# Kernel optimization log

Hardware: AMD Instinct MI355X
Metric: run time of the kernel (lower is better)

Reference implementation:

```python
import jax, jax.numpy as jnp
import numpy as np

N_P, N_A, D, E = 200000, 100000, 256, 1000000


def setup_inputs() -> dict:
    key = jax.random.key(0)
    ks = jax.random.split(key, 6)
    return {
        "x_paper": jax.random.normal(ks[0], (N_P, D), dtype=jnp.float32),
        "x_author": jax.random.normal(ks[1], (N_A, D), dtype=jnp.float32),
        # relation ('paper','to','author'): src in [0,N_P), dst in [0,N_A)
        "e_pa_src": jax.random.randint(ks[2], (E,), 0, N_P),
        "e_pa_dst": jax.random.randint(ks[3], (E,), 0, N_A),
        # relation ('author','to','paper'): src in [0,N_A), dst in [0,N_P)
        "e_ap_src": jax.random.randint(ks[4], (E,), 0, N_A),
        "e_ap_dst": jax.random.randint(ks[5], (E,), 0, N_P),
    }


def reference(x_paper, x_author, e_pa_src, e_pa_dst, e_ap_src, e_ap_dst):
    n_author = x_author.shape[0]  # x_dict['author'] supplies dst size for hop 1
    n_paper = x_paper.shape[0]
    # Hop 1: conv over ('paper','to','author'): gather x_paper at edge src,
    # scatter-sum to author dst, then per-dict relu (norm=False => plain x_j messages).
    x_a1 = jax.nn.relu(
        jax.ops.segment_sum(x_paper[e_pa_src], e_pa_dst, num_segments=n_author)
    )
    # Hop 2: conv over ('author','to','paper') reads the updated author features.
    x_p2 = jax.nn.relu(
        jax.ops.segment_sum(x_a1[e_ap_src], e_ap_dst, num_segments=n_paper)
    )
    # collect_mode=False -> return x_dict[metapath[0]] == updated paper features
    return x_p2
```

## Files before the change

kernel.cpp:

```cpp
#include <hip/hip_runtime.h>

#define DIM 256
#define RPB 32
#define LOG_RPB 5
#define NG 8
#define BATCH 16
#define CAP 128
#define BCAP 512
#define PC_B 3072

typedef float f32x4 __attribute__((ext_vector_type(4)));
typedef unsigned int u32;
typedef unsigned short u16;

__device__ __forceinline__ u16 f32_to_bf16_rne(float f) {
    u32 u = __float_as_uint(f);
    return (u16)((u + 0x7FFFu + ((u >> 16) & 1u)) >> 16);
}


__global__ void place_conv(const int* __restrict__ sA, const int* __restrict__ dA,
                           const int* __restrict__ sB, const int* __restrict__ dB,
                           int* __restrict__ cnt, u32* __restrict__ binned,
                           int TBc, int NBA_, int E1, int Etot,
                           const float* __restrict__ xin, u16* __restrict__ xbf,
                           long long n4) {
    int sub = ((int)blockIdx.x >> 4) * 8 + ((int)blockIdx.x & 7);
    int half = (int)gridDim.x >> 1;
    if ((((int)blockIdx.x >> 3) & 1) == 0) {
        int stride = half * (int)blockDim.x;
        for (int e = sub * (int)blockDim.x + (int)threadIdx.x; e < Etot; e += stride) {
            int g = (e >> 8) & (NG - 1);
            int s, d, b;
            if (e < E1) {
                s = __builtin_nontemporal_load(sA + e);
                d = __builtin_nontemporal_load(dA + e);
                b = d >> LOG_RPB;
            } else {
                int e2 = e - E1;
                s = __builtin_nontemporal_load(sB + e2);
                d = __builtin_nontemporal_load(dB + e2);
                b = NBA_ + (d >> LOG_RPB);
            }
            int cell = g * TBc + b;
            int old = atomicAdd(&cnt[cell], 1);
            if (old < CAP)
                binned[(long long)cell * CAP + old] = ((u32)s << LOG_RPB) | (u32)(d & (RPB - 1));
        }
    } else {
        long long stride = (long long)half * blockDim.x;
        for (long long i = (long long)sub * blockDim.x + threadIdx.x; i < n4; i += stride) {
            f32x4 v = __builtin_nontemporal_load((const f32x4*)xin + i);
            ushort4 o;
            o.x = f32_to_bf16_rne(v.x); o.y = f32_to_bf16_rne(v.y);
            o.z = f32_to_bf16_rne(v.z); o.w = f32_to_bf16_rne(v.w);
            *((ushort4*)xbf + i) = o;
        }
    }
}


__global__ void local_sort(const u32* __restrict__ binned, const int* __restrict__ cnt,
                           int* __restrict__ sorted, int* __restrict__ rp33, int TBc) {
    __shared__ int c[RPB];
    __shared__ int cur[RPB];
    int b = blockIdx.x;
    int tid = threadIdx.x;
    if (tid < RPB) c[tid] = 0;
    __syncthreads();
#pragma unroll
    for (int g = 0; g < NG; ++g) {
        int cell = g * TBc + b;
        int n = cnt[cell]; n = (n < CAP) ? n : CAP;
        long long base = (long long)cell * CAP;
        for (int i = tid; i < n; i += (int)blockDim.x)
            atomicAdd(&c[binned[base + i] & (RPB - 1)], 1);
    }
    __syncthreads();
    if (tid == 0) {
        int run = b * BCAP;
        for (int r = 0; r < RPB; ++r) {
            cur[r] = run;
            rp33[b * 33 + r] = run;
            run += c[r];
        }
        rp33[b * 33 + RPB] = run;
    }
    __syncthreads();
#pragma unroll
    for (int g = 0; g < NG; ++g) {
        int cell = g * TBc + b;
        int n = cnt[cell]; n = (n < CAP) ? n : CAP;
        long long base = (long long)cell * CAP;
        for (int i = tid; i < n; i += (int)blockDim.x) {
            u32 e = binned[base + i];
            int pos = atomicAdd(&cur[e & (RPB - 1)], 1);
            sorted[pos] = (int)(e >> LOG_RPB);
        }
    }
}


template <bool DBF>
__global__ void gather_rows(const u16* __restrict__ xv,
                            const int* __restrict__ rp33,
                            const int* __restrict__ sorted_src,
                            void* __restrict__ outv, int n) {
    int gtid = blockIdx.x * blockDim.x + threadIdx.x;
    int r = gtid >> 6;
    int lane = gtid & 63;
    if (r >= n) return;
    int bi = (r >> LOG_RPB) * 33 + (r & (RPB - 1));
    int beg = rp33[bi];
    int end = rp33[bi + 1];
    float ax = 0.f, ay = 0.f, az = 0.f, aw = 0.f;
    for (int i = beg; i < end; i += BATCH) {
        int cnt = end - i;
        cnt = (cnt < BATCH) ? cnt : BATCH;
        int li = (lane < cnt) ? lane : (cnt - 1);
        int sid = sorted_src[i + li];
#pragma unroll
        for (int j = 0; j < BATCH; ++j) {
            if (j >= cnt) break;
            int s = __builtin_amdgcn_readlane(sid, j);
            const uint2* row = (const uint2*)(xv + (long long)s * DIM);
            uint2 v = row[lane];
            ax += __uint_as_float(v.x << 16);
            ay += __uint_as_float(v.x & 0xFFFF0000u);
            az += __uint_as_float(v.y << 16);
            aw += __uint_as_float(v.y & 0xFFFF0000u);
        }
    }
    ax = fmaxf(ax, 0.f); ay = fmaxf(ay, 0.f); az = fmaxf(az, 0.f); aw = fmaxf(aw, 0.f);
    if (DBF) {
        ushort4 o;
        o.x = f32_to_bf16_rne(ax); o.y = f32_to_bf16_rne(ay);
        o.z = f32_to_bf16_rne(az); o.w = f32_to_bf16_rne(aw);
        *((ushort4*)outv + (long long)r * (DIM / 4) + lane) = o;
    } else {
        f32x4 o = { ax, ay, az, aw };
        __builtin_nontemporal_store(o, (f32x4*)outv + (long long)r * (DIM / 4) + lane);
    }
}


extern "C" void kernel_launch(void* const* d_in, const int* in_sizes, int n_in,
                              void* d_out, int out_size, void* d_ws, size_t ws_size,
                              hipStream_t stream) {
    const float* x_paper = (const float*)d_in[0];
    const int* e_pa_src = (const int*)d_in[2];
    const int* e_pa_dst = (const int*)d_in[3];
    const int* e_ap_src = (const int*)d_in[4];
    const int* e_ap_dst = (const int*)d_in[5];

    const int nA = in_sizes[1] / DIM;
    const int nB = in_sizes[0] / DIM;
    const int E1 = in_sizes[2];
    const int E2 = in_sizes[4];
    const int Etot = E1 + E2;

    const int NBA = (nA + RPB - 1) / RPB;
    const int NBB = (nB + RPB - 1) / RPB;
    const int TBc = NBA + NBB;

    size_t off = 0;
    auto alloc = [&](size_t bytes) { size_t o = off; off += (bytes + 255) & ~(size_t)255; return o; };
    size_t o_xpbf   = alloc((size_t)nB * DIM * sizeof(u16));
    size_t o_xa1    = alloc((size_t)nA * DIM * sizeof(u16));
    size_t o_cnt    = alloc((size_t)NG * TBc * sizeof(int));
    size_t o_binned = alloc((size_t)NG * TBc * CAP * sizeof(u32));
    size_t o_sorted = alloc((size_t)TBc * BCAP * sizeof(int));
    size_t o_rp33   = alloc(((size_t)TBc * 33 + 1) * sizeof(int));
    (void)ws_size;

    char* ws = (char*)d_ws;
    u16* xpbf   = (u16*)(ws + o_xpbf);
    u16* x_a1   = (u16*)(ws + o_xa1);
    int* cnt    = (int*)(ws + o_cnt);
    u32* binned = (u32*)(ws + o_binned);
    int* sorted = (int*)(ws + o_sorted);
    int* rp33   = (int*)(ws + o_rp33);
    float* x_p2 = (float*)d_out;

    hipMemsetAsync(cnt, 0, (size_t)NG * TBc * sizeof(int), stream);

    long long n4 = (long long)nB * DIM / 4;
    place_conv<<<PC_B, 256, 0, stream>>>(
        e_pa_src, e_pa_dst, e_ap_src, e_ap_dst, cnt, binned,
        TBc, NBA, E1, Etot, x_paper, xpbf, n4);

    local_sort<<<TBc, 256, 0, stream>>>(binned, cnt, sorted, rp33, TBc);

    gather_rows<true><<<(nA + 3) / 4, 256, 0, stream>>>(
        xpbf, rp33, sorted, x_a1, nA);
    gather_rows<false><<<(nB + 3) / 4, 256, 0, stream>>>(
        x_a1, rp33 + (size_t)NBA * 33, sorted, x_p2, nB);
}
```

Baseline: 318.6 us.

## Overlap hop-2 bucket sort with hop-1 gather and batch gather loads

Splits the local sort into a relation-A launch and a combined launch where relation-B bucket sorting runs in the same grid as the hop-1 row gather, so the two independent phases share the GPU. The place kernel now has every block do both edge binning and the bf16 conversion instead of splitting blocks between the two roles. The gather inner loop issues all BATCH row loads up front and masks the accumulation instead of breaking early, exposing more memory-level parallelism. The cost is redundant loads of the last valid row for short batches and a less specialized place kernel.

```diff
diff --git a/kernel.cpp b/kernel.cpp
--- a/kernel.cpp
+++ b/kernel.cpp
@@ -25,11 +25,10 @@
                            int TBc, int NBA_, int E1, int Etot,
                            const float* __restrict__ xin, u16* __restrict__ xbf,
                            long long n4) {
-    int sub = ((int)blockIdx.x >> 4) * 8 + ((int)blockIdx.x & 7);
-    int half = (int)gridDim.x >> 1;
-    if ((((int)blockIdx.x >> 3) & 1) == 0) {
-        int stride = half * (int)blockDim.x;
-        for (int e = sub * (int)blockDim.x + (int)threadIdx.x; e < Etot; e += stride) {
+    {
+        int stride = (int)gridDim.x * (int)blockDim.x;
+        for (int e = (int)blockIdx.x * (int)blockDim.x + (int)threadIdx.x;
+             e < Etot; e += stride) {
             int g = (e >> 8) & (NG - 1);
             int s, d, b;
             if (e < E1) {
@@ -47,9 +46,11 @@
             if (old < CAP)
                 binned[(long long)cell * CAP + old] = ((u32)s << LOG_RPB) | (u32)(d & (RPB - 1));
         }
-    } else {
-        long long stride = (long long)half * blockDim.x;
-        for (long long i = (long long)sub * blockDim.x + threadIdx.x; i < n4; i += stride) {
+    }
+    {
+        long long stride = (long long)gridDim.x * blockDim.x;
+        for (long long i = (long long)blockIdx.x * blockDim.x + threadIdx.x;
+             i < n4; i += stride) {
             f32x4 v = __builtin_nontemporal_load((const f32x4*)xin + i);
             ushort4 o;
             o.x = f32_to_bf16_rne(v.x); o.y = f32_to_bf16_rne(v.y);
@@ -60,11 +61,12 @@
 }
 
 
-__global__ void local_sort(const u32* __restrict__ binned, const int* __restrict__ cnt,
-                           int* __restrict__ sorted, int* __restrict__ rp33, int TBc) {
+__device__ __forceinline__ void sort_bucket(int b, const u32* __restrict__ binned,
+                                            const int* __restrict__ cnt,
+                                            int* __restrict__ sorted,
+                                            int* __restrict__ rp33, int TBc) {
     __shared__ int c[RPB];
     __shared__ int cur[RPB];
-    int b = blockIdx.x;
     int tid = threadIdx.x;
     if (tid < RPB) c[tid] = 0;
     __syncthreads();
@@ -73,7 +75,7 @@
         int cell = g * TBc + b;
         int n = cnt[cell]; n = (n < CAP) ? n : CAP;
         long long base = (long long)cell * CAP;
-        for (int i = tid; i < n; i += (int)blockDim.x)
+        for (int i = tid; i < n; i += 256)
             atomicAdd(&c[binned[base + i] & (RPB - 1)], 1);
     }
     __syncthreads();
@@ -92,7 +94,7 @@
         int cell = g * TBc + b;
         int n = cnt[cell]; n = (n < CAP) ? n : CAP;
         long long base = (long long)cell * CAP;
-        for (int i = tid; i < n; i += (int)blockDim.x) {
+        for (int i = tid; i < n; i += 256) {
             u32 e = binned[base + i];
             int pos = atomicAdd(&cur[e & (RPB - 1)], 1);
             sorted[pos] = (int)(e >> LOG_RPB);
@@ -100,13 +102,18 @@
     }
 }
 
+__global__ void local_sortA(const u32* __restrict__ binned, const int* __restrict__ cnt,
+                            int* __restrict__ sorted, int* __restrict__ rp33, int TBc) {
+    sort_bucket(blockIdx.x, binned, cnt, sorted, rp33, TBc);
+}
+
 
 template <bool DBF>
-__global__ void gather_rows(const u16* __restrict__ xv,
-                            const int* __restrict__ rp33,
-                            const int* __restrict__ sorted_src,
-                            void* __restrict__ outv, int n) {
-    int gtid = blockIdx.x * blockDim.x + threadIdx.x;
+__device__ __forceinline__ void gather_body(const u16* __restrict__ xv,
+                                            const int* __restrict__ rp33,
+                                            const int* __restrict__ sorted_src,
+                                            void* __restrict__ outv, int n, int blk) {
+    int gtid = blk * 256 + (int)threadIdx.x;
     int r = gtid >> 6;
     int lane = gtid & 63;
     if (r >= n) return;
@@ -119,16 +126,19 @@
         cnt = (cnt < BATCH) ? cnt : BATCH;
         int li = (lane < cnt) ? lane : (cnt - 1);
         int sid = sorted_src[i + li];
+        uint2 vv[BATCH];
 #pragma unroll
         for (int j = 0; j < BATCH; ++j) {
-            if (j >= cnt) break;
             int s = __builtin_amdgcn_readlane(sid, j);
-            const uint2* row = (const uint2*)(xv + (long long)s * DIM);
-            uint2 v = row[lane];
-            ax += __uint_as_float(v.x << 16);
-            ay += __uint_as_float(v.x & 0xFFFF0000u);
-            az += __uint_as_float(v.y << 16);
-            aw += __uint_as_float(v.y & 0xFFFF0000u);
+            vv[j] = *((const uint2*)(xv + (long long)s * DIM) + lane);
+        }
+#pragma unroll
+        for (int j = 0; j < BATCH; ++j) {
+            float m = (j < cnt) ? 1.0f : 0.0f;
+            ax = fmaf(m, __uint_as_float(vv[j].x << 16), ax);
+            ay = fmaf(m, __uint_as_float(vv[j].x & 0xFFFF0000u), ay);
+            az = fmaf(m, __uint_as_float(vv[j].y << 16), az);
+            aw = fmaf(m, __uint_as_float(vv[j].y & 0xFFFF0000u), aw);
         }
     }
     ax = fmaxf(ax, 0.f); ay = fmaxf(ay, 0.f); az = fmaxf(az, 0.f); aw = fmaxf(aw, 0.f);
@@ -144,6 +154,23 @@
 }
 
 
+__global__ void sortB_gather1(const u32* __restrict__ binned, const int* __restrict__ cnt,
+                              int* __restrict__ sorted, int* __restrict__ rp33, int TBc,
+                              int NBA_, int NBB_,
+                              const u16* __restrict__ xpbf, u16* __restrict__ x_a1, int nA) {
+    if ((int)blockIdx.x < NBB_) {
+        sort_bucket(NBA_ + (int)blockIdx.x, binned, cnt, sorted, rp33, TBc);
+        return;
+    }
+    gather_body<true>(xpbf, rp33, sorted, x_a1, nA, (int)blockIdx.x - NBB_);
+}
+
+__global__ void gather2(const u16* __restrict__ x_a1, const int* __restrict__ rp33B,
+                        const int* __restrict__ sorted, float* __restrict__ x_p2, int nB) {
+    gather_body<false>(x_a1, rp33B, sorted, x_p2, nB, (int)blockIdx.x);
+}
+
+
 extern "C" void kernel_launch(void* const* d_in, const int* in_sizes, int n_in,
                               void* d_out, int out_size, void* d_ws, size_t ws_size,
                               hipStream_t stream) {
@@ -189,10 +216,11 @@
         e_pa_src, e_pa_dst, e_ap_src, e_ap_dst, cnt, binned,
         TBc, NBA, E1, Etot, x_paper, xpbf, n4);
 
-    local_sort<<<TBc, 256, 0, stream>>>(binned, cnt, sorted, rp33, TBc);
-
-    gather_rows<true><<<(nA + 3) / 4, 256, 0, stream>>>(
-        xpbf, rp33, sorted, x_a1, nA);
-    gather_rows<false><<<(nB + 3) / 4, 256, 0, stream>>>(
+    local_sortA<<<NBA, 256, 0, stream>>>(binned, cnt, sorted, rp33, TBc);
+
+    sortB_gather1<<<NBB + (nA + 3) / 4, 256, 0, stream>>>(
+        binned, cnt, sorted, rp33, TBc, NBA, NBB, xpbf, x_a1, nA);
+
+    gather2<<<(nB + 3) / 4, 256, 0, stream>>>(
         x_a1, rp33 + (size_t)NBA * 33, sorted, x_p2, nB);
 }
```

Result: slower. 347.9 us (+9.2%).

## Fuse per-bucket local sort into gather kernels using shared-memory sorted lists

Applied to the files above, without the earlier changes.

Merges the separate local_sort kernel into each hop's gather kernel. Each block now counting-sorts its 32-row bucket's edges into shared memory and then gathers rows directly from LDS, which removes the global sorted/rp33 arrays and one launch. The gather loop also now issues all 16 row loads before accumulating, using masked FMAs instead of an early break, to raise memory-level parallelism. The costs are one block handling 32 rows with only 4 waves, which lowers parallelism per row, and redundant loads of clamped duplicate indices in partial batches.

```diff
diff --git a/kernel.cpp b/kernel.cpp
--- a/kernel.cpp
+++ b/kernel.cpp
@@ -60,86 +60,86 @@
 }
 
 
-__global__ void local_sort(const u32* __restrict__ binned, const int* __restrict__ cnt,
-                           int* __restrict__ sorted, int* __restrict__ rp33, int TBc) {
+template <bool DBF>
+__global__ void __launch_bounds__(256)
+gather_hop(const u32* __restrict__ binned, const int* __restrict__ cnt,
+           const u16* __restrict__ xv, void* __restrict__ outv,
+           int TBc, int bucket_base, int n) {
+    __shared__ int sed[BCAP];
+    __shared__ int rp[RPB + 1];
     __shared__ int c[RPB];
     __shared__ int cur[RPB];
-    int b = blockIdx.x;
-    int tid = threadIdx.x;
+
+    int tid = (int)threadIdx.x;
+    int b = bucket_base + (int)blockIdx.x;
+
     if (tid < RPB) c[tid] = 0;
     __syncthreads();
 #pragma unroll
     for (int g = 0; g < NG; ++g) {
         int cell = g * TBc + b;
-        int n = cnt[cell]; n = (n < CAP) ? n : CAP;
+        int m = cnt[cell]; m = (m < CAP) ? m : CAP;
         long long base = (long long)cell * CAP;
-        for (int i = tid; i < n; i += (int)blockDim.x)
+        for (int i = tid; i < m; i += 256)
             atomicAdd(&c[binned[base + i] & (RPB - 1)], 1);
     }
     __syncthreads();
     if (tid == 0) {
-        int run = b * BCAP;
-        for (int r = 0; r < RPB; ++r) {
-            cur[r] = run;
-            rp33[b * 33 + r] = run;
-            run += c[r];
-        }
-        rp33[b * 33 + RPB] = run;
+        int run = 0;
+        for (int r = 0; r < RPB; ++r) { cur[r] = run; rp[r] = run; run += c[r]; }
+        rp[RPB] = run;
     }
     __syncthreads();
 #pragma unroll
     for (int g = 0; g < NG; ++g) {
         int cell = g * TBc + b;
-        int n = cnt[cell]; n = (n < CAP) ? n : CAP;
+        int m = cnt[cell]; m = (m < CAP) ? m : CAP;
         long long base = (long long)cell * CAP;
-        for (int i = tid; i < n; i += (int)blockDim.x) {
+        for (int i = tid; i < m; i += 256) {
             u32 e = binned[base + i];
             int pos = atomicAdd(&cur[e & (RPB - 1)], 1);
-            sorted[pos] = (int)(e >> LOG_RPB);
+            sed[pos] = (int)(e >> LOG_RPB);
         }
     }
-}
+    __syncthreads();
 
-
-template <bool DBF>
-__global__ void gather_rows(const u16* __restrict__ xv,
-                            const int* __restrict__ rp33,
-                            const int* __restrict__ sorted_src,
-                            void* __restrict__ outv, int n) {
-    int gtid = blockIdx.x * blockDim.x + threadIdx.x;
-    int r = gtid >> 6;
-    int lane = gtid & 63;
-    if (r >= n) return;
-    int bi = (r >> LOG_RPB) * 33 + (r & (RPB - 1));
-    int beg = rp33[bi];
-    int end = rp33[bi + 1];
-    float ax = 0.f, ay = 0.f, az = 0.f, aw = 0.f;
-    for (int i = beg; i < end; i += BATCH) {
-        int cnt = end - i;
-        cnt = (cnt < BATCH) ? cnt : BATCH;
-        int li = (lane < cnt) ? lane : (cnt - 1);
-        int sid = sorted_src[i + li];
+    int lane = tid & 63, w = tid >> 6;
+    int row0 = (int)blockIdx.x * RPB;
+    for (int rr = w; rr < RPB; rr += 4) {
+        int row = row0 + rr;
+        if (row >= n) break;
+        int beg = rp[rr];
+        int end = rp[rr + 1];
+        float ax = 0.f, ay = 0.f, az = 0.f, aw = 0.f;
+        for (int i = beg; i < end; i += BATCH) {
+            int m = end - i;
+            m = (m < BATCH) ? m : BATCH;
+            uint2 vv[BATCH];
 #pragma unroll
-        for (int j = 0; j < BATCH; ++j) {
-            if (j >= cnt) break;
-            int s = __builtin_amdgcn_readlane(sid, j);
-            const uint2* row = (const uint2*)(xv + (long long)s * DIM);
-            uint2 v = row[lane];
-            ax += __uint_as_float(v.x << 16);
-            ay += __uint_as_float(v.x & 0xFFFF0000u);
-            az += __uint_as_float(v.y << 16);
-            aw += __uint_as_float(v.y & 0xFFFF0000u);
+            for (int j = 0; j < BATCH; ++j) {
+                int jj = (j < m) ? j : (m - 1);
+                int s = sed[i + jj];
+                vv[j] = *((const uint2*)(xv + (long long)s * DIM) + lane);
+            }
+#pragma unroll
+            for (int j = 0; j < BATCH; ++j) {
+                float mk = (j < m) ? 1.0f : 0.0f;
+                ax = fmaf(mk, __uint_as_float(vv[j].x << 16), ax);
+                ay = fmaf(mk, __uint_as_float(vv[j].x & 0xFFFF0000u), ay);
+                az = fmaf(mk, __uint_as_float(vv[j].y << 16), az);
+                aw = fmaf(mk, __uint_as_float(vv[j].y & 0xFFFF0000u), aw);
+            }
         }
-    }
-    ax = fmaxf(ax, 0.f); ay = fmaxf(ay, 0.f); az = fmaxf(az, 0.f); aw = fmaxf(aw, 0.f);
-    if (DBF) {
-        ushort4 o;
-        o.x = f32_to_bf16_rne(ax); o.y = f32_to_bf16_rne(ay);
-        o.z = f32_to_bf16_rne(az); o.w = f32_to_bf16_rne(aw);
-        *((ushort4*)outv + (long long)r * (DIM / 4) + lane) = o;
-    } else {
-        f32x4 o = { ax, ay, az, aw };
-        __builtin_nontemporal_store(o, (f32x4*)outv + (long long)r * (DIM / 4) + lane);
+        ax = fmaxf(ax, 0.f); ay = fmaxf(ay, 0.f); az = fmaxf(az, 0.f); aw = fmaxf(aw, 0.f);
+        if (DBF) {
+            ushort4 o;
+            o.x = f32_to_bf16_rne(ax); o.y = f32_to_bf16_rne(ay);
+            o.z = f32_to_bf16_rne(az); o.w = f32_to_bf16_rne(aw);
+            *((ushort4*)outv + (long long)row * (DIM / 4) + lane) = o;
+        } else {
+            f32x4 o = { ax, ay, az, aw };
+            __builtin_nontemporal_store(o, (f32x4*)outv + (long long)row * (DIM / 4) + lane);
+        }
     }
 }
 
@@ -169,8 +169,6 @@
     size_t o_xa1    = alloc((size_t)nA * DIM * sizeof(u16));
     size_t o_cnt    = alloc((size_t)NG * TBc * sizeof(int));
     size_t o_binned = alloc((size_t)NG * TBc * CAP * sizeof(u32));
-    size_t o_sorted = alloc((size_t)TBc * BCAP * sizeof(int));
-    size_t o_rp33   = alloc(((size_t)TBc * 33 + 1) * sizeof(int));
     (void)ws_size;
 
     char* ws = (char*)d_ws;
@@ -178,8 +176,6 @@
     u16* x_a1   = (u16*)(ws + o_xa1);
     int* cnt    = (int*)(ws + o_cnt);
     u32* binned = (u32*)(ws + o_binned);
-    int* sorted = (int*)(ws + o_sorted);
-    int* rp33   = (int*)(ws + o_rp33);
     float* x_p2 = (float*)d_out;
 
     hipMemsetAsync(cnt, 0, (size_t)NG * TBc * sizeof(int), stream);
@@ -189,10 +185,7 @@
         e_pa_src, e_pa_dst, e_ap_src, e_ap_dst, cnt, binned,
         TBc, NBA, E1, Etot, x_paper, xpbf, n4);
 
-    local_sort<<<TBc, 256, 0, stream>>>(binned, cnt, sorted, rp33, TBc);
+    gather_hop<true><<<NBA, 256, 0, stream>>>(binned, cnt, xpbf, x_a1, TBc, 0, nA);
 
-    gather_rows<true><<<(nA + 3) / 4, 256, 0, stream>>>(
-        xpbf, rp33, sorted, x_a1, nA);
-    gather_rows<false><<<(nB + 3) / 4, 256, 0, stream>>>(
-        x_a1, rp33 + (size_t)NBA * 33, sorted, x_p2, nB);
+    gather_hop<false><<<NBB, 256, 0, stream>>>(binned, cnt, x_a1, x_p2, TBc, NBA, nB);
 }
```

After: 303.0 us. -4.9%, faster.
